# Kernel optimization log

Measured on AMD Instinct MI355X. Metric: run time of the kernel, lower is better.

## Reference

```python
import jax, jax.numpy as jnp
import numpy as np

N = 20000      # nodes
E = 320000     # edges (avg degree 16)
G = 256        # graphs
F_NODE = 64
F_EDGE = 16
HID = 256
H, C = 4, 64   # heads, per-head channels
EPS = 1e-5


def setup_inputs() -> dict:
    key = jax.random.key(0)
    ks = jax.random.split(key, 24)
    def rn(k, shape, scale=0.05):
        return jax.random.normal(k, shape, dtype=jnp.float32) * scale
    src = jax.random.randint(ks[0], (E,), 0, N)
    dst = (src + 1 + jax.random.randint(ks[1], (E,), 0, N - 1)) % N  # no pre-existing self loops
    edge_index = jnp.stack([src, dst]).astype(jnp.int32)
    batch = ((jnp.arange(N) * G) // N).astype(jnp.int32)  # contiguous graph ids, all G graphs non-empty
    return {
        'x': rn(ks[2], (N, F_NODE), 1.0),
        'edge_index': edge_index,
        'batch': batch,
        'edge_attr': rn(ks[3], (E, F_EDGE), 1.0),
        'enc_W': rn(ks[4], (F_NODE, HID)),
        'enc_b': jnp.zeros((HID,), jnp.float32),
        'conv_Wl': rn(ks[5], (3, HID, HID)),
        'conv_bl': rn(ks[6], (3, HID)),
        'conv_Wr': rn(ks[7], (3, HID, HID)),
        'conv_br': rn(ks[8], (3, HID)),
        'conv_We': rn(ks[9], (3, F_EDGE, HID)),
        'conv_att': rn(ks[10], (3, H, C)),
        'conv_bias': rn(ks[11], (3, HID)),
        'bn_gamma': jnp.ones((3, HID), jnp.float32),
        'bn_beta': jnp.zeros((3, HID), jnp.float32),
        'bn_mean': rn(ks[12], (3, HID)),
        'bn_var': jax.random.uniform(ks[13], (3, HID), dtype=jnp.float32) + 0.5,
        'cls_W1': rn(ks[14], (2 * HID, HID)),
        'cls_b1': jnp.zeros((HID,), jnp.float32),
        'cls_g1': jnp.ones((HID,), jnp.float32),
        'cls_bt1': jnp.zeros((HID,), jnp.float32),
        'cls_m1': rn(ks[15], (HID,)),
        'cls_v1': jax.random.uniform(ks[16], (HID,), dtype=jnp.float32) + 0.5,
        'cls_W2': rn(ks[17], (HID, HID // 2)),
        'cls_b2': jnp.zeros((HID // 2,), jnp.float32),
        'cls_g2': jnp.ones((HID // 2,), jnp.float32),
        'cls_bt2': jnp.zeros((HID // 2,), jnp.float32),
        'cls_m2': rn(ks[18], (HID // 2,)),
        'cls_v2': jax.random.uniform(ks[19], (HID // 2,), dtype=jnp.float32) + 0.5,
        'cls_W3': rn(ks[20], (HID // 2, 1)),
        'cls_b3': jnp.zeros((1,), jnp.float32),
    }


def _bn(v, g, b, m, var):
    return (v - m) * jax.lax.rsqrt(var + EPS) * g + b


def _gatv2(h, src, dst, eattr, Wl, bl, Wr, br, We, att, bias, n):
    # GATv2Conv (share_weights=False, concat=True) with edge features.
    xl = (h @ Wl + bl).reshape(n, H, C)          # messages come from lin_l(source)
    xr = (h @ Wr + br).reshape(n, H, C)
    ef = (eattr @ We).reshape(-1, H, C)
    z = jax.nn.leaky_relu(xl[src] + xr[dst] + ef, 0.2)   # [E', H, C]
    alpha = jnp.einsum('ehc,hc->eh', z, att)             # [E', H]
    amax = jax.ops.segment_max(alpha, dst, num_segments=n)
    amax = jnp.where(jnp.isfinite(amax), amax, 0.0)
    ex = jnp.exp(alpha - amax[dst])
    den = jax.ops.segment_sum(ex, dst, num_segments=n)
    a = ex / den[dst]                                    # self loops guarantee den > 0
    out = jax.ops.segment_sum(a[:, :, None] * xl[src], dst, num_segments=n)
    return out.reshape(n, H * C) + bias


def reference(x, edge_index, batch, edge_attr, enc_W, enc_b, conv_Wl, conv_bl, conv_Wr, conv_br, conv_We, conv_att, conv_bias, bn_gamma, bn_beta, bn_mean, bn_var, cls_W1, cls_b1, cls_g1, cls_bt1, cls_m1, cls_v1, cls_W2, cls_b2, cls_g2, cls_bt2, cls_m2, cls_v2, cls_W3, cls_b3):
    n = x.shape[0]
    src, dst = edge_index[0], edge_index[1]
    # add self loops with fill_value='mean' (mean of incoming edge_attr per node)
    deg = jax.ops.segment_sum(jnp.ones(src.shape, x.dtype), dst, num_segments=n)
    loop_attr = jax.ops.segment_sum(edge_attr, dst, num_segments=n) / jnp.maximum(deg, 1.0)[:, None]
    loop = jnp.arange(n, dtype=src.dtype)
    src2 = jnp.concatenate([src, loop])
    dst2 = jnp.concatenate([dst, loop])
    ea2 = jnp.concatenate([edge_attr, loop_attr], axis=0)

    h = jax.nn.relu(x @ enc_W + enc_b)
    for i in range(3):  # fixed layer count
        h_in = h
        hc = _gatv2(h, src2, dst2, ea2, conv_Wl[i], conv_bl[i], conv_Wr[i], conv_br[i], conv_We[i], conv_att[i], conv_bias[i], n)
        h = jax.nn.relu(_bn(hc, bn_gamma[i], bn_beta[i], bn_mean[i], bn_var[i])) + h_in

    cnt = jax.ops.segment_sum(jnp.ones((n,), h.dtype), batch, num_segments=G)
    x_mean = jax.ops.segment_sum(h, batch, num_segments=G) / jnp.maximum(cnt, 1.0)[:, None]
    x_max = jax.ops.segment_max(h, batch, num_segments=G)
    xp = jnp.concatenate([x_mean, x_max], axis=1)

    z = jax.nn.relu(_bn(xp @ cls_W1 + cls_b1, cls_g1, cls_bt1, cls_m1, cls_v1))
    z = jax.nn.relu(_bn(z @ cls_W2 + cls_b2, cls_g2, cls_bt2, cls_m2, cls_v2))
    return (z @ cls_W3 + cls_b3)[:, 0]
```

## Files before the change

### kernel.cpp

```cpp
#include <hip/hip_runtime.h>
#include <hip/hip_bf16.h>

#define N_NODES 20000
#define N_EDGES 320000
#define N_E2    (N_EDGES + N_NODES)
#define N_GRAPHS 256
#define HID 256
#define EPS 1e-5f
#define NSCAN 20
#define CPB 8

typedef unsigned short u16;
typedef __attribute__((ext_vector_type(8))) short short8;
typedef __attribute__((ext_vector_type(4))) float f32x4;

__device__ __forceinline__ float b2f(u16 u) {
    union { unsigned int i; float f; } v; v.i = ((unsigned int)u) << 16; return v.f;
}
__device__ __forceinline__ u16 f2b(float f) {
    __hip_bfloat16 h = __float2bfloat16(f);
    return *reinterpret_cast<u16*>(&h);
}

__global__ void k_init(int* cnt, int* cursor) {
    int i = blockIdx.x * 256 + threadIdx.x;
    if (i < N_NODES) { cnt[i] = 1; cursor[i] = 0; }
}

__global__ void k_count(const int* __restrict__ dst, int* __restrict__ cnt) {
    int e = blockIdx.x * 256 + threadIdx.x;
    if (e < N_EDGES) atomicAdd(&cnt[dst[e]], 1);
}

__global__ void k_scan1(const int* __restrict__ cnt, int* __restrict__ rowp, int* __restrict__ part) {
    __shared__ int ls[256];
    int b = blockIdx.x, tid = threadIdx.x;
    int base = b * 1024 + tid * 4;
    int c[4]; int s = 0;
#pragma unroll
    for (int u = 0; u < 4; u++) { int i = base + u; c[u] = (i < N_NODES) ? cnt[i] : 0; s += c[u]; }
    ls[tid] = s; __syncthreads();
    for (int off = 1; off < 256; off <<= 1) {
        int v = (tid >= off) ? ls[tid - off] : 0;
        __syncthreads();
        ls[tid] += v;
        __syncthreads();
    }
    int excl = ls[tid] - s;
#pragma unroll
    for (int u = 0; u < 4; u++) { int i = base + u; if (i < N_NODES) rowp[i] = excl; excl += c[u]; }
    if (tid == 255) part[b] = ls[255];
}

__global__ void k_scan2(int* part, int* rowp) {
    int s = 0;
    for (int b = 0; b < NSCAN; b++) { int v = part[b]; part[b] = s; s += v; }
    rowp[N_NODES] = s;
}

__global__ void k_scan3(int* __restrict__ rowp, const int* __restrict__ part) {
    int b = blockIdx.x, tid = threadIdx.x;
    int add = part[b];
    int base = b * 1024 + tid * 4;
#pragma unroll
    for (int u = 0; u < 4; u++) { int i = base + u; if (i < N_NODES) rowp[i] += add; }
}

__global__ void k_fill(const int* __restrict__ src, const int* __restrict__ dst,
                       const int* __restrict__ rowp, int* __restrict__ cursor,
                       int* __restrict__ csr_src, int* __restrict__ csr_dst,
                       int* __restrict__ csr_aid) {
    int t = blockIdx.x * 256 + threadIdx.x;
    if (t < N_EDGES) {
        int d = dst[t];
        int pos = atomicAdd(&cursor[d], 1);
        int w = rowp[d] + pos;
        csr_src[w] = src[t];
        csr_dst[w] = d;
        csr_aid[w] = t;
    } else if (t < N_E2) {
        int n = t - N_EDGES;
        int pos = atomicAdd(&cursor[n], 1);
        int w = rowp[n] + pos;
        csr_src[w] = n;
        csr_dst[w] = n;
        csr_aid[w] = N_EDGES + n;
    }
}

__global__ void k_pad(int* csr_src, int* csr_dst) {
    int i = threadIdx.x;
    csr_src[N_E2 + i] = 0;
    csr_dst[N_E2 + i] = 0;
}

__global__ void k_loopattr(const int* __restrict__ rowp, const int* __restrict__ csr_aid,
                           const float* __restrict__ edge_attr, float* __restrict__ lattr) {
    int t = blockIdx.x * 256 + threadIdx.x;
    if (t >= N_NODES * 16) return;
    int n = t >> 4, j = t & 15;
    int st = rowp[n], en = rowp[n + 1];
    float s = 0.f;
    for (int i = st; i < en; i++) {
        int aid = csr_aid[i];
        if (aid < N_EDGES) s += edge_attr[(size_t)aid * 16 + j];
    }
    float deg = (float)(en - st - 1);
    lattr[(size_t)n * 16 + j] = s / fmaxf(deg, 1.0f);
}

__global__ void k_eacsr(const int* __restrict__ csr_aid,
                        const float* __restrict__ edge_attr,
                        const float* __restrict__ lattr,
                        u16* __restrict__ ea_bf) {
    int t = blockIdx.x * 256 + threadIdx.x;
    if (t >= N_E2 * 2) return;
    int e = t >> 1, hf = t & 1;
    int aid = csr_aid[e];
    const float* ap = (aid < N_EDGES) ? edge_attr + (size_t)aid * 16
                                      : lattr + (size_t)(aid - N_EDGES) * 16;
    float4 a = ((const float4*)ap)[hf * 2];
    float4 b = ((const float4*)ap)[hf * 2 + 1];
    u16 v[8] = {f2b(a.x), f2b(a.y), f2b(a.z), f2b(a.w),
                f2b(b.x), f2b(b.y), f2b(b.z), f2b(b.w)};
    *(uint4*)(ea_bf + (size_t)t * 8) = *(uint4*)v;
}

__global__ void k_wef(const float* __restrict__ We, u16* __restrict__ Wef) {
    int t = blockIdx.x * 256 + threadIdx.x;
    if (t >= 3 * 16 * 64) return;
    int layer = t >> 10, r = t & 1023;
    int nt = r >> 6, l = r & 63;
    int kc = l >> 4, ch = nt * 16 + (l & 15);
    u16 v[8];
#pragma unroll
    for (int q = 0; q < 8; q++) {
        float x = 0.f;
        if (kc < 2) x = We[(size_t)layer * 4096 + (size_t)(kc * 8 + q) * 256 + ch];
        v[q] = f2b(x);
    }
    *(uint4*)(Wef + (size_t)t * 8) = *(uint4*)v;
}

__global__ void k_xbf(const float* __restrict__ x, u16* __restrict__ xb) {
    int t = blockIdx.x * 256 + threadIdx.x;
    if (t >= N_NODES * 16) return;
    float4 v = ((const float4*)x)[t];
    u16 o[4] = {f2b(v.x), f2b(v.y), f2b(v.z), f2b(v.w)};
    *(ushort4*)(xb + (size_t)t * 4) = *(ushort4*)o;
}

__global__ void k_twg(const float* __restrict__ W, u16* __restrict__ Wt, int K, int N) {
    __shared__ float tile[32][33];
    int layer = blockIdx.z;
    const float* Wp = W + (size_t)layer * K * N;
    u16* Wtp = Wt + (size_t)layer * K * N;
    int bk = blockIdx.x * 32, bn = blockIdx.y * 32;
    int tx = threadIdx.x & 31, ty = threadIdx.x >> 5;
#pragma unroll
    for (int q = 0; q < 4; q++) {
        int k = bk + ty + q * 8;
        tile[ty + q * 8][tx] = Wp[(size_t)k * N + bn + tx];
    }
    __syncthreads();
#pragma unroll
    for (int q = 0; q < 4; q++) {
        int n = bn + ty + q * 8;
        Wtp[(size_t)n * K + bk + tx] = f2b(tile[tx][ty + q * 8]);
    }
}

template <int EPI>
__global__ __launch_bounds__(256) void k_gemm_bf(
    const u16* __restrict__ A, int lda,
    const u16* __restrict__ Bt, int ldb, int K,
    const float* __restrict__ bias,
    u16* __restrict__ Cbf, int ldc, int coff,
    float* __restrict__ Cf, int M)
{
    __shared__ __align__(16) u16 As[128 * 40];
    __shared__ __align__(16) u16 Bs[64 * 40];
    int tid = threadIdx.x;
    int lane = tid & 63, w = tid >> 6;
    int m0 = blockIdx.x * 128, n0 = blockIdx.y * 64;

    f32x4 acc[2][4];
#pragma unroll
    for (int i = 0; i < 2; i++)
#pragma unroll
        for (int j = 0; j < 4; j++) acc[i][j] = (f32x4){0.f, 0.f, 0.f, 0.f};

    int srow = tid >> 2, skc = (tid & 3) * 8;
    int lr = lane & 15, lk = (lane >> 4) * 8;

    int ktiles = K >> 5;
    for (int kt = 0; kt < ktiles; kt++) {
        if (kt) __syncthreads();
#pragma unroll
        for (int q = 0; q < 2; q++) {
            int arow = q * 64 + srow;
            uint4 av = make_uint4(0, 0, 0, 0);
            if (m0 + arow < M)
                av = *(const uint4*)(A + (size_t)(m0 + arow) * lda + kt * 32 + skc);
            *(uint4*)&As[arow * 40 + skc] = av;
        }
        {
            uint4 bv = *(const uint4*)(Bt + (size_t)(n0 + srow) * ldb + kt * 32 + skc);
            *(uint4*)&Bs[srow * 40 + skc] = bv;
        }
        __syncthreads();

        short8 af0 = *(const short8*)&As[(w * 32 + lr) * 40 + lk];
        short8 af1 = *(const short8*)&As[(w * 32 + 16 + lr) * 40 + lk];
        short8 bf[4];
#pragma unroll
        for (int nt = 0; nt < 4; nt++)
            bf[nt] = *(const short8*)&Bs[(nt * 16 + lr) * 40 + lk];
#pragma unroll
        for (int nt = 0; nt < 4; nt++) {
            acc[0][nt] = __builtin_amdgcn_mfma_f32_16x16x32_bf16(af0, bf[nt], acc[0][nt], 0, 0, 0);
            acc[1][nt] = __builtin_amdgcn_mfma_f32_16x16x32_bf16(af1, bf[nt], acc[1][nt], 0, 0, 0);
        }
    }

    int rq = (lane >> 4) * 4;
#pragma unroll
    for (int nt = 0; nt < 4; nt++) {
        int col = n0 + nt * 16 + lr;
        float bv = bias[col];
#pragma unroll
        for (int mt = 0; mt < 2; mt++) {
#pragma unroll
            for (int j = 0; j < 4; j++) {
                int row = m0 + w * 32 + mt * 16 + rq + j;
                if (row < M) {
                    float v = acc[mt][nt][j] + bv;
                    if (EPI == 1) {
                        v = fmaxf(v, 0.f);
                        Cf[(size_t)row * ldc + col] = v;
                        Cbf[(size_t)row * ldc + col] = f2b(v);
                    } else {
                        Cbf[(size_t)row * ldc + coff + col] = f2b(v);
                    }
                }
            }
        }
    }
}

__global__ __launch_bounds__(256) void k_alpha3(
    const u16* __restrict__ xlr,
    const u16* __restrict__ ea_bf,
    const int* __restrict__ csr_src, const int* __restrict__ csr_dst,
    const u16* __restrict__ Wef,
    const float* __restrict__ att,
    float* __restrict__ alpha)
{
    __shared__ __align__(16) u16 wef_s[16 * 64 * 8];
    int tid = threadIdx.x, lane = tid & 63, w = tid >> 6;
    {
        const uint4* s = (const uint4*)Wef;
        uint4* d = (uint4*)wef_s;
#pragma unroll
        for (int q = 0; q < 4; q++) d[q * 256 + tid] = s[q * 256 + tid];
    }
    int eg = lane >> 4, t16 = lane & 15;

    float att_r[16];
#pragma unroll
    for (int q = 0; q < 16; q++) att_r[q] = att[q * 16 + t16];
    __syncthreads();

    for (int it = 0; it < CPB; it++) {
        int chunk = blockIdx.x * CPB + it;
        if (chunk * 64 >= N_E2) break;
        int e_base = chunk * 64 + w * 16;

        short8 afrag = {0, 0, 0, 0, 0, 0, 0, 0};
        if (eg < 2) {
            int e = e_base + t16; if (e > N_E2 - 1) e = N_E2 - 1;
            afrag = *(const short8*)(ea_bf + (size_t)e * 16 + eg * 8);
        }
        int4 s4 = *(const int4*)(csr_src + e_base + eg * 4);
        int4 d4 = *(const int4*)(csr_dst + e_base + eg * 4);
        const u16* xlp[4]; const u16* xrp[4];
        xlp[0] = xlr + (size_t)s4.x * 512;       xlp[1] = xlr + (size_t)s4.y * 512;
        xlp[2] = xlr + (size_t)s4.z * 512;       xlp[3] = xlr + (size_t)s4.w * 512;
        xrp[0] = xlr + (size_t)d4.x * 512 + 256; xrp[1] = xlr + (size_t)d4.y * 512 + 256;
        xrp[2] = xlr + (size_t)d4.z * 512 + 256; xrp[3] = xlr + (size_t)d4.w * 512 + 256;

        float pj[4] = {0.f, 0.f, 0.f, 0.f};
#pragma unroll
        for (int nt = 0; nt < 16; nt++) {
            short8 bfrag = *(const short8*)&wef_s[(nt * 64 + lane) * 8];
            f32x4 D = __builtin_amdgcn_mfma_f32_16x16x32_bf16(
                afrag, bfrag, (f32x4){0.f, 0.f, 0.f, 0.f}, 0, 0, 0);
            int ch = nt * 16 + t16;
#pragma unroll
            for (int j = 0; j < 4; j++) {
                float z = D[j] + b2f(xlp[j][ch]) + b2f(xrp[j][ch]);
                z = fmaxf(z, 0.f) + 0.2f * fminf(z, 0.f);
                pj[j] = fmaf(z, att_r[nt], pj[j]);
            }
            if ((nt & 3) == 3) {
                int hh = nt >> 2;
#pragma unroll
                for (int j = 0; j < 4; j++) {
                    float p = pj[j];
                    p += __shfl_xor(p, 1, 64);
                    p += __shfl_xor(p, 2, 64);
                    p += __shfl_xor(p, 4, 64);
                    p += __shfl_xor(p, 8, 64);
                    int e = e_base + eg * 4 + j;
                    if (t16 == 0 && e < N_E2) alpha[(size_t)e * 4 + hh] = p;
                    pj[j] = 0.f;
                }
            }
        }
    }
}

__global__ __launch_bounds__(256) void k_aggr(
    const u16* __restrict__ xlr, const float* __restrict__ alpha,
    const int* __restrict__ rowp, const int* __restrict__ csr_src,
    const float* __restrict__ cbias,
    const float* __restrict__ bng, const float* __restrict__ bnb,
    const float* __restrict__ bnm, const float* __restrict__ bnv,
    float* __restrict__ h, u16* __restrict__ h_bf)
{
    __shared__ float lex[4][64][4];
    __shared__ int   lsrc[4][64];
    int lane = threadIdx.x & 63;
    int wv = threadIdx.x >> 6;
    int n = blockIdx.x * 4 + wv;
    if (n >= N_NODES) return;
    int st = rowp[n], en = rowp[n + 1];
    int hsel = lane >> 4;
    int c0 = lane * 4;

    float m4[4]  = {-3.0e38f, -3.0e38f, -3.0e38f, -3.0e38f};
    float den4[4] = {0.f, 0.f, 0.f, 0.f};
    float acc[4]  = {0.f, 0.f, 0.f, 0.f};

    for (int cs = st; cs < en; cs += 64) {
        int cnt = min(64, en - cs);
        float a4[4];
        int s_i = 0;
        if (lane < cnt) {
            float4 v = *(const float4*)(alpha + (size_t)(cs + lane) * 4);
            a4[0] = v.x; a4[1] = v.y; a4[2] = v.z; a4[3] = v.w;
            s_i = csr_src[cs + lane];
        } else {
            a4[0] = a4[1] = a4[2] = a4[3] = -3.0e38f;
        }
        float cm[4] = {a4[0], a4[1], a4[2], a4[3]};
#pragma unroll
        for (int o = 32; o >= 1; o >>= 1)
#pragma unroll
            for (int u = 0; u < 4; u++) cm[u] = fmaxf(cm[u], __shfl_xor(cm[u], o, 64));
        float sc[4];
#pragma unroll
        for (int u = 0; u < 4; u++) {
            float nm = fmaxf(m4[u], cm[u]);
            sc[u] = __expf(m4[u] - nm);
            den4[u] *= sc[u];
            m4[u] = nm;
        }
        float scl = sc[hsel];
#pragma unroll
        for (int u = 0; u < 4; u++) acc[u] *= scl;
        float ex[4];
#pragma unroll
        for (int u = 0; u < 4; u++) ex[u] = (lane < cnt) ? __expf(a4[u] - m4[u]) : 0.f;
        float sx[4] = {ex[0], ex[1], ex[2], ex[3]};
#pragma unroll
        for (int o = 32; o >= 1; o >>= 1)
#pragma unroll
            for (int u = 0; u < 4; u++) sx[u] += __shfl_xor(sx[u], o, 64);
#pragma unroll
        for (int u = 0; u < 4; u++) den4[u] += sx[u];
        *(float4*)&lex[wv][lane][0] = make_float4(ex[0], ex[1], ex[2], ex[3]);
        lsrc[wv][lane] = s_i;
        int j = 0;
        for (; j + 8 <= cnt; j += 8) {
            float a[8]; int sj[8];
#pragma unroll
            for (int q = 0; q < 8; q++) { a[q] = lex[wv][j + q][hsel]; sj[q] = lsrc[wv][j + q]; }
            ushort4 xg[8];
#pragma unroll
            for (int q = 0; q < 8; q++) xg[q] = *(const ushort4*)(xlr + (size_t)sj[q] * 512 + c0);
#pragma unroll
            for (int q = 0; q < 8; q++) {
                acc[0] += a[q] * b2f(((const u16*)&xg[q])[0]);
                acc[1] += a[q] * b2f(((const u16*)&xg[q])[1]);
                acc[2] += a[q] * b2f(((const u16*)&xg[q])[2]);
                acc[3] += a[q] * b2f(((const u16*)&xg[q])[3]);
            }
        }
        for (; j < cnt; j++) {
            float a = lex[wv][j][hsel];
            int sj = lsrc[wv][j];
            ushort4 xg = *(const ushort4*)(xlr + (size_t)sj * 512 + c0);
            acc[0] += a * b2f(((const u16*)&xg)[0]);
            acc[1] += a * b2f(((const u16*)&xg)[1]);
            acc[2] += a * b2f(((const u16*)&xg)[2]);
            acc[3] += a * b2f(((const u16*)&xg)[3]);
        }
    }

    float dd = den4[hsel];
    float4 hin = *(const float4*)(h + (size_t)n * 256 + c0);
    float4 cb  = *(const float4*)(cbias + c0);
    float4 gg  = *(const float4*)(bng + c0);
    float4 bb  = *(const float4*)(bnb + c0);
    float4 mm  = *(const float4*)(bnm + c0);
    float4 vv  = *(const float4*)(bnv + c0);
    float hi[4] = {hin.x, hin.y, hin.z, hin.w};
    float cbv[4] = {cb.x, cb.y, cb.z, cb.w};
    float gv[4] = {gg.x, gg.y, gg.z, gg.w};
    float bv[4] = {bb.x, bb.y, bb.z, bb.w};
    float mv[4] = {mm.x, mm.y, mm.z, mm.w};
    float vvv[4] = {vv.x, vv.y, vv.z, vv.w};
    float4 o;
    ushort4 ob;
#pragma unroll
    for (int u = 0; u < 4; u++) {
        float val = acc[u] / dd + cbv[u];
        val = (val - mv[u]) * rsqrtf(vvv[u] + EPS) * gv[u] + bv[u];
        val = fmaxf(val, 0.f) + hi[u];
        ((float*)&o)[u] = val;
        ((u16*)&ob)[u] = f2b(val);
    }
    *(float4*)(h + (size_t)n * 256 + c0) = o;
    *(ushort4*)(h_bf + (size_t)n * 256 + c0) = ob;
}

__global__ __launch_bounds__(256) void k_head(
    const float* __restrict__ h,
    const float* __restrict__ W1, const float* __restrict__ b1,
    const float* __restrict__ g1, const float* __restrict__ bt1,
    const float* __restrict__ m1, const float* __restrict__ v1,
    const float* __restrict__ W2, const float* __restrict__ b2,
    const float* __restrict__ g2, const float* __restrict__ bt2,
    const float* __restrict__ m2, const float* __restrict__ v2,
    const float* __restrict__ W3, const float* __restrict__ b3,
    float* __restrict__ out)
{
    __shared__ float xp_s[512];
    __shared__ float z1_s[256];
    __shared__ float z2_s[128];
    int g = blockIdx.x, c = threadIdx.x;
    int st = (g * N_NODES + N_GRAPHS - 1) / N_GRAPHS;
    int en = ((g + 1) * N_NODES + N_GRAPHS - 1) / N_GRAPHS;

    float s = 0.f, mx = -3.0e38f;
    for (int i = st; i < en; i++) {
        float v = h[(size_t)i * 256 + c];
        s += v;
        mx = fmaxf(mx, v);
    }
    xp_s[c] = s / (float)(en - st);
    xp_s[256 + c] = mx;
    __syncthreads();

    float a = 0.f;
#pragma unroll 8
    for (int k = 0; k < 512; k++) a = fmaf(xp_s[k], W1[k * 256 + c], a);
    a += b1[c];
    a = (a - m1[c]) * rsqrtf(v1[c] + EPS) * g1[c] + bt1[c];
    z1_s[c] = fmaxf(a, 0.f);
    __syncthreads();

    if (c < 128) {
        float a2 = 0.f;
#pragma unroll 8
        for (int k = 0; k < 256; k++) a2 = fmaf(z1_s[k], W2[k * 128 + c], a2);
        a2 += b2[c];
        a2 = (a2 - m2[c]) * rsqrtf(v2[c] + EPS) * g2[c] + bt2[c];
        z2_s[c] = fmaxf(a2, 0.f);
    }
    __syncthreads();

    if (c < 64) {
        float a3 = z2_s[c] * W3[c] + z2_s[c + 64] * W3[c + 64];
#pragma unroll
        for (int o = 32; o >= 1; o >>= 1) a3 += __shfl_xor(a3, o, 64);
        if (c == 0) out[g] = a3 + b3[0];
    }
}

extern "C" void kernel_launch(void* const* d_in, const int* in_sizes, int n_in,
                              void* d_out, int out_size, void* d_ws, size_t ws_size,
                              hipStream_t stream) {
    const float* x         = (const float*)d_in[0];
    const int*   ei        = (const int*)d_in[1];
    const int*   src       = ei;
    const int*   dst       = ei + N_EDGES;
    const float* edge_attr = (const float*)d_in[3];
    const float* enc_W     = (const float*)d_in[4];
    const float* enc_b     = (const float*)d_in[5];
    const float* conv_Wl   = (const float*)d_in[6];
    const float* conv_bl   = (const float*)d_in[7];
    const float* conv_Wr   = (const float*)d_in[8];
    const float* conv_br   = (const float*)d_in[9];
    const float* conv_We   = (const float*)d_in[10];
    const float* conv_att  = (const float*)d_in[11];
    const float* conv_bias = (const float*)d_in[12];
    const float* bn_g      = (const float*)d_in[13];
    const float* bn_b      = (const float*)d_in[14];
    const float* bn_m      = (const float*)d_in[15];
    const float* bn_v      = (const float*)d_in[16];
    const float* cls_W1    = (const float*)d_in[17];
    const float* cls_b1    = (const float*)d_in[18];
    const float* cls_g1    = (const float*)d_in[19];
    const float* cls_bt1   = (const float*)d_in[20];
    const float* cls_m1    = (const float*)d_in[21];
    const float* cls_v1    = (const float*)d_in[22];
    const float* cls_W2    = (const float*)d_in[23];
    const float* cls_b2    = (const float*)d_in[24];
    const float* cls_g2    = (const float*)d_in[25];
    const float* cls_bt2   = (const float*)d_in[26];
    const float* cls_m2    = (const float*)d_in[27];
    const float* cls_v2    = (const float*)d_in[28];
    const float* cls_W3    = (const float*)d_in[29];
    const float* cls_b3    = (const float*)d_in[30];
    float* out = (float*)d_out;

    char* ws = (char*)d_ws;
    size_t off = 0;
    auto alloc = [&](size_t bytes) -> void* {
        void* p = ws + off;
        off += (bytes + 255) & ~(size_t)255;
        return p;
    };
    float* h       = (float*)alloc((size_t)N_NODES * 256 * 4);
    u16*   h_bf    = (u16*)alloc((size_t)N_NODES * 256 * 2);
    u16*   xlr_bf  = (u16*)alloc((size_t)N_NODES * 512 * 2);
    float* lattr   = (float*)alloc((size_t)N_NODES * 16 * 4);
    u16*   ea_bf   = (u16*)alloc((size_t)N_E2 * 16 * 2);
    float* alphas  = (float*)alloc((size_t)N_E2 * 4 * 4);
    u16*   x_bf    = (u16*)alloc((size_t)N_NODES * 64 * 2);
    u16*   enc_Wt  = (u16*)alloc((size_t)64 * 256 * 2);
    u16*   Wtl     = (u16*)alloc((size_t)3 * 65536 * 2);
    u16*   Wtr     = (u16*)alloc((size_t)3 * 65536 * 2);
    u16*   Wef     = (u16*)alloc((size_t)3 * 16 * 64 * 8 * 2);
    int*   cnt     = (int*)alloc((size_t)N_NODES * 4);
    int*   rowp    = (int*)alloc((size_t)(N_NODES + 1) * 4);
    int*   cursor  = (int*)alloc((size_t)N_NODES * 4);
    int*   csr_src = (int*)alloc((size_t)(N_E2 + 512) * 4);
    int*   csr_dst = (int*)alloc((size_t)(N_E2 + 512) * 4);
    int*   csr_aid = (int*)alloc((size_t)N_E2 * 4);
    int*   part    = (int*)alloc(64 * 4);

    k_init<<<(N_NODES + 255) / 256, 256, 0, stream>>>(cnt, cursor);
    k_count<<<(N_EDGES + 255) / 256, 256, 0, stream>>>(dst, cnt);
    k_scan1<<<NSCAN, 256, 0, stream>>>(cnt, rowp, part);
    k_scan2<<<1, 1, 0, stream>>>(part, rowp);
    k_scan3<<<NSCAN, 256, 0, stream>>>(rowp, part);
    k_fill<<<(N_E2 + 255) / 256, 256, 0, stream>>>(src, dst, rowp, cursor, csr_src, csr_dst, csr_aid);
    k_pad<<<1, 512, 0, stream>>>(csr_src, csr_dst);
    k_loopattr<<<(N_NODES * 16 + 255) / 256, 256, 0, stream>>>(rowp, csr_aid, edge_attr, lattr);
    k_eacsr<<<(N_E2 * 2 + 255) / 256, 256, 0, stream>>>(csr_aid, edge_attr, lattr, ea_bf);

    k_xbf<<<(N_NODES * 16 + 255) / 256, 256, 0, stream>>>(x, x_bf);
    k_twg<<<dim3(2, 8, 1), 256, 0, stream>>>(enc_W, enc_Wt, 64, 256);
    k_twg<<<dim3(8, 8, 3), 256, 0, stream>>>(conv_Wl, Wtl, 256, 256);
    k_twg<<<dim3(8, 8, 3), 256, 0, stream>>>(conv_Wr, Wtr, 256, 256);
    k_wef<<<12, 256, 0, stream>>>(conv_We, Wef);

    dim3 ggrid((N_NODES + 127) / 128, 4);
    k_gemm_bf<1><<<ggrid, 256, 0, stream>>>(x_bf, 64, enc_Wt, 64, 64,
                                            enc_b, h_bf, 256, 0, h, N_NODES);

    int nchunks = (N_E2 + 63) / 64;
    int ablocks = (nchunks + CPB - 1) / CPB;
    for (int i = 0; i < 3; i++) {
        k_gemm_bf<0><<<ggrid, 256, 0, stream>>>(h_bf, 256, Wtl + (size_t)i * 65536, 256, 256,
                                                conv_bl + i * HID, xlr_bf, 512, 0, nullptr, N_NODES);
        k_gemm_bf<0><<<ggrid, 256, 0, stream>>>(h_bf, 256, Wtr + (size_t)i * 65536, 256, 256,
                                                conv_br + i * HID, xlr_bf, 512, 256, nullptr, N_NODES);
        k_alpha3<<<ablocks, 256, 0, stream>>>(
            xlr_bf, ea_bf, csr_src, csr_dst,
            Wef + (size_t)i * 8192, conv_att + (size_t)i * 256, alphas);
        k_aggr<<<N_NODES / 4, 256, 0, stream>>>(
            xlr_bf, alphas, rowp, csr_src,
            conv_bias + (size_t)i * HID,
            bn_g + (size_t)i * HID, bn_b + (size_t)i * HID,
            bn_m + (size_t)i * HID, bn_v + (size_t)i * HID, h, h_bf);
    }

    k_head<<<N_GRAPHS, 256, 0, stream>>>(
        h, cls_W1, cls_b1, cls_g1, cls_bt1, cls_m1, cls_v1,
        cls_W2, cls_b2, cls_g2, cls_bt2, cls_m2, cls_v2,
        cls_W3, cls_b3, out);
}
```

Before: 496.3 us.

## Transpose alpha MFMA to vectorize gathers and split graph pooling across blocks

Measured after the change: 496.2 us. No clear change (-0.0%).

```diff
diff --git a/kernel.cpp b/kernel.cpp
--- a/kernel.cpp
+++ b/kernel.cpp
@@ -257,64 +257,53 @@
     float* __restrict__ alpha)
 {
     __shared__ __align__(16) u16 wef_s[16 * 64 * 8];
+    __shared__ float att_s[256];
     int tid = threadIdx.x, lane = tid & 63, w = tid >> 6;
     {
         const uint4* s = (const uint4*)Wef;
         uint4* d = (uint4*)wef_s;
 #pragma unroll
         for (int q = 0; q < 4; q++) d[q * 256 + tid] = s[q * 256 + tid];
+        att_s[tid] = att[tid];
     }
     int eg = lane >> 4, t16 = lane & 15;
-
-    float att_r[16];
-#pragma unroll
-    for (int q = 0; q < 16; q++) att_r[q] = att[q * 16 + t16];
     __syncthreads();
 
     for (int it = 0; it < CPB; it++) {
         int chunk = blockIdx.x * CPB + it;
         if (chunk * 64 >= N_E2) break;
         int e_base = chunk * 64 + w * 16;
-
-        short8 afrag = {0, 0, 0, 0, 0, 0, 0, 0};
-        if (eg < 2) {
-            int e = e_base + t16; if (e > N_E2 - 1) e = N_E2 - 1;
-            afrag = *(const short8*)(ea_bf + (size_t)e * 16 + eg * 8);
-        }
-        int4 s4 = *(const int4*)(csr_src + e_base + eg * 4);
-        int4 d4 = *(const int4*)(csr_dst + e_base + eg * 4);
-        const u16* xlp[4]; const u16* xrp[4];
-        xlp[0] = xlr + (size_t)s4.x * 512;       xlp[1] = xlr + (size_t)s4.y * 512;
-        xlp[2] = xlr + (size_t)s4.z * 512;       xlp[3] = xlr + (size_t)s4.w * 512;
-        xrp[0] = xlr + (size_t)d4.x * 512 + 256; xrp[1] = xlr + (size_t)d4.y * 512 + 256;
-        xrp[2] = xlr + (size_t)d4.z * 512 + 256; xrp[3] = xlr + (size_t)d4.w * 512 + 256;
-
-        float pj[4] = {0.f, 0.f, 0.f, 0.f};
+        int e_raw = e_base + t16;
+        int e = (e_raw < N_E2) ? e_raw : N_E2 - 1;
+
+        short8 eafrag = {0, 0, 0, 0, 0, 0, 0, 0};
+        if (eg < 2) eafrag = *(const short8*)(ea_bf + (size_t)e * 16 + eg * 8);
+        int s = csr_src[e], d = csr_dst[e];
+        const u16* xlp = xlr + (size_t)s * 512;
+        const u16* xrp = xlr + (size_t)d * 512 + 256;
+
+        float pj = 0.f;
 #pragma unroll
         for (int nt = 0; nt < 16; nt++) {
-            short8 bfrag = *(const short8*)&wef_s[(nt * 64 + lane) * 8];
+            short8 wfrag = *(const short8*)&wef_s[(nt * 64 + lane) * 8];
             f32x4 D = __builtin_amdgcn_mfma_f32_16x16x32_bf16(
-                afrag, bfrag, (f32x4){0.f, 0.f, 0.f, 0.f}, 0, 0, 0);
-            int ch = nt * 16 + t16;
+                wfrag, eafrag, (f32x4){0.f, 0.f, 0.f, 0.f}, 0, 0, 0);
+            int ch0 = nt * 16 + eg * 4;
+            ushort4 xl4 = *(const ushort4*)(xlp + ch0);
+            ushort4 xr4 = *(const ushort4*)(xrp + ch0);
+            float4 at4 = *(const float4*)&att_s[ch0];
 #pragma unroll
             for (int j = 0; j < 4; j++) {
-                float z = D[j] + b2f(xlp[j][ch]) + b2f(xrp[j][ch]);
+                float z = D[j] + b2f(((const u16*)&xl4)[j]) + b2f(((const u16*)&xr4)[j]);
                 z = fmaxf(z, 0.f) + 0.2f * fminf(z, 0.f);
-                pj[j] = fmaf(z, att_r[nt], pj[j]);
+                pj = fmaf(z, ((const float*)&at4)[j], pj);
             }
             if ((nt & 3) == 3) {
-                int hh = nt >> 2;
-#pragma unroll
-                for (int j = 0; j < 4; j++) {
-                    float p = pj[j];
-                    p += __shfl_xor(p, 1, 64);
-                    p += __shfl_xor(p, 2, 64);
-                    p += __shfl_xor(p, 4, 64);
-                    p += __shfl_xor(p, 8, 64);
-                    int e = e_base + eg * 4 + j;
-                    if (t16 == 0 && e < N_E2) alpha[(size_t)e * 4 + hh] = p;
-                    pj[j] = 0.f;
-                }
+                float p = pj;
+                p += __shfl_xor(p, 16, 64);
+                p += __shfl_xor(p, 32, 64);
+                if (eg == 0 && e_raw < N_E2) alpha[(size_t)e_raw * 4 + (nt >> 2)] = p;
+                pj = 0.f;
             }
         }
     }
@@ -435,8 +424,27 @@
     *(ushort4*)(h_bf + (size_t)n * 256 + c0) = ob;
 }
 
+__global__ __launch_bounds__(256) void k_poolp(
+    const float* __restrict__ h, float* __restrict__ psum, float* __restrict__ pmax)
+{
+    int g = blockIdx.x, p = blockIdx.y, c = threadIdx.x;
+    int gst = (g * N_NODES + N_GRAPHS - 1) / N_GRAPHS;
+    int gen = ((g + 1) * N_NODES + N_GRAPHS - 1) / N_GRAPHS;
+    int len = gen - gst;
+    int cst = gst + (len * p) / 8;
+    int cen = gst + (len * (p + 1)) / 8;
+    float s = 0.f, mx = -3.0e38f;
+    for (int i = cst; i < cen; i++) {
+        float v = h[(size_t)i * 256 + c];
+        s += v;
+        mx = fmaxf(mx, v);
+    }
+    psum[(size_t)(g * 8 + p) * 256 + c] = s;
+    pmax[(size_t)(g * 8 + p) * 256 + c] = mx;
+}
+
 __global__ __launch_bounds__(256) void k_head(
-    const float* __restrict__ h,
+    const float* __restrict__ psum, const float* __restrict__ pmax,
     const float* __restrict__ W1, const float* __restrict__ b1,
     const float* __restrict__ g1, const float* __restrict__ bt1,
     const float* __restrict__ m1, const float* __restrict__ v1,
@@ -448,44 +456,58 @@
 {
     __shared__ float xp_s[512];
     __shared__ float z1_s[256];
+    __shared__ float z2p[2][128];
     __shared__ float z2_s[128];
     int g = blockIdx.x, c = threadIdx.x;
-    int st = (g * N_NODES + N_GRAPHS - 1) / N_GRAPHS;
-    int en = ((g + 1) * N_NODES + N_GRAPHS - 1) / N_GRAPHS;
+    int gst = (g * N_NODES + N_GRAPHS - 1) / N_GRAPHS;
+    int gen = ((g + 1) * N_NODES + N_GRAPHS - 1) / N_GRAPHS;
 
     float s = 0.f, mx = -3.0e38f;
-    for (int i = st; i < en; i++) {
-        float v = h[(size_t)i * 256 + c];
-        s += v;
-        mx = fmaxf(mx, v);
-    }
-    xp_s[c] = s / (float)(en - st);
+#pragma unroll
+    for (int p = 0; p < 8; p++) {
+        s += psum[(size_t)(g * 8 + p) * 256 + c];
+        mx = fmaxf(mx, pmax[(size_t)(g * 8 + p) * 256 + c]);
+    }
+    xp_s[c] = s / (float)(gen - gst);
     xp_s[256 + c] = mx;
     __syncthreads();
 
-    float a = 0.f;
-#pragma unroll 8
-    for (int k = 0; k < 512; k++) a = fmaf(xp_s[k], W1[k * 256 + c], a);
-    a += b1[c];
+    float a0 = 0.f, a1 = 0.f, a2 = 0.f, a3 = 0.f;
+#pragma unroll 4
+    for (int k = 0; k < 512; k += 4) {
+        a0 = fmaf(xp_s[k + 0], W1[(k + 0) * 256 + c], a0);
+        a1 = fmaf(xp_s[k + 1], W1[(k + 1) * 256 + c], a1);
+        a2 = fmaf(xp_s[k + 2], W1[(k + 2) * 256 + c], a2);
+        a3 = fmaf(xp_s[k + 3], W1[(k + 3) * 256 + c], a3);
+    }
+    float a = (a0 + a1) + (a2 + a3) + b1[c];
     a = (a - m1[c]) * rsqrtf(v1[c] + EPS) * g1[c] + bt1[c];
     z1_s[c] = fmaxf(a, 0.f);
     __syncthreads();
 
+    {
+        int c2 = c & 127, half = c >> 7;
+        float b_acc = 0.f;
+#pragma unroll 4
+        for (int k = 0; k < 128; k++) {
+            int kk = half * 128 + k;
+            b_acc = fmaf(z1_s[kk], W2[kk * 128 + c2], b_acc);
+        }
+        z2p[half][c2] = b_acc;
+    }
+    __syncthreads();
     if (c < 128) {
-        float a2 = 0.f;
-#pragma unroll 8
-        for (int k = 0; k < 256; k++) a2 = fmaf(z1_s[k], W2[k * 128 + c], a2);
-        a2 += b2[c];
-        a2 = (a2 - m2[c]) * rsqrtf(v2[c] + EPS) * g2[c] + bt2[c];
-        z2_s[c] = fmaxf(a2, 0.f);
+        float a2v = z2p[0][c] + z2p[1][c] + b2[c];
+        a2v = (a2v - m2[c]) * rsqrtf(v2[c] + EPS) * g2[c] + bt2[c];
+        z2_s[c] = fmaxf(a2v, 0.f);
     }
     __syncthreads();
 
     if (c < 64) {
-        float a3 = z2_s[c] * W3[c] + z2_s[c + 64] * W3[c + 64];
-#pragma unroll
-        for (int o = 32; o >= 1; o >>= 1) a3 += __shfl_xor(a3, o, 64);
-        if (c == 0) out[g] = a3 + b3[0];
+        float a3v = z2_s[c] * W3[c] + z2_s[c + 64] * W3[c + 64];
+#pragma unroll
+        for (int o = 32; o >= 1; o >>= 1) a3v += __shfl_xor(a3v, o, 64);
+        if (c == 0) out[g] = a3v + b3[0];
     }
 }
 
@@ -544,6 +566,8 @@
     u16*   Wtl     = (u16*)alloc((size_t)3 * 65536 * 2);
     u16*   Wtr     = (u16*)alloc((size_t)3 * 65536 * 2);
     u16*   Wef     = (u16*)alloc((size_t)3 * 16 * 64 * 8 * 2);
+    float* psum    = (float*)alloc((size_t)N_GRAPHS * 8 * 256 * 4);
+    float* pmax    = (float*)alloc((size_t)N_GRAPHS * 8 * 256 * 4);
     int*   cnt     = (int*)alloc((size_t)N_NODES * 4);
     int*   rowp    = (int*)alloc((size_t)(N_NODES + 1) * 4);
     int*   cursor  = (int*)alloc((size_t)N_NODES * 4);
@@ -589,8 +613,9 @@
             bn_m + (size_t)i * HID, bn_v + (size_t)i * HID, h, h_bf);
     }
 
+    k_poolp<<<dim3(N_GRAPHS, 8), 256, 0, stream>>>(h, psum, pmax);
     k_head<<<N_GRAPHS, 256, 0, stream>>>(
-        h, cls_W1, cls_b1, cls_g1, cls_bt1, cls_m1, cls_v1,
+        psum, pmax, cls_W1, cls_b1, cls_g1, cls_bt1, cls_m1, cls_v1,
         cls_W2, cls_b2, cls_g2, cls_bt2, cls_m2, cls_v2,
         cls_W3, cls_b3, out);
 }
```
